# Kernel tuning notes

Measured on AMD Instinct MI355X. Metric: run time of the kernel, lower is better.

## Reference

```python
import jax, jax.numpy as jnp
import numpy as np

B, S, D, H = 2, 2048, 1024, 16
DK = D // H  # 64
THETA = 10000.0
SCALE = 1.0 / np.sqrt(DK)


def _rope(t, pos):
    """Apply rotary embedding. t: [b,h,s,dk], pos: [b,s] int."""
    inv_freq = THETA ** (-jnp.arange(0, DK, 2, dtype=jnp.float32) / DK)  # [dk/2]
    ang = pos[:, None, :, None].astype(jnp.float32) * inv_freq  # [b,1,s,dk/2]
    cos, sin = jnp.cos(ang), jnp.sin(ang)
    t1, t2 = t[..., 0::2], t[..., 1::2]  # interleaved pairs
    rot = jnp.stack([t1 * cos - t2 * sin, t1 * sin + t2 * cos], axis=-1)
    return rot.reshape(t.shape)


def setup_inputs() -> dict:
    key = jax.random.key(0)
    ks = jax.random.split(key, 9)
    sc = 0.02
    x = jax.random.normal(ks[0], (B, S, D), jnp.float32)
    token_position = jnp.tile(jnp.arange(S, dtype=jnp.int32)[None, :], (B, 1))
    Wq = jax.random.normal(ks[1], (D, D), jnp.float32) * sc
    Wk = jax.random.normal(ks[2], (D, D), jnp.float32) * sc
    Wv = jax.random.normal(ks[3], (D, D), jnp.float32) * sc
    Wo = jax.random.normal(ks[4], (D, D), jnp.float32) * sc
    bq = jnp.zeros((D,), jnp.float32)
    bk = jnp.zeros((D,), jnp.float32)
    bv = jnp.zeros((D,), jnp.float32)
    bo = jnp.zeros((D,), jnp.float32)
    return {"x": x, "token_position": token_position,
            "Wq": Wq, "bq": bq, "Wk": Wk, "bk": bk,
            "Wv": Wv, "bv": bv, "Wo": Wo, "bo": bo}


def reference(x, token_position, Wq, bq, Wk, bk, Wv, bv, Wo, bo):
    b, s, d = x.shape
    # projections, split heads: [b,s,d] -> [b,h,s,dk]
    def heads(t):
        return t.reshape(b, s, H, DK).transpose(0, 2, 1, 3)
    q = heads(x @ Wq + bq)
    k = heads(x @ Wk + bk)
    v = heads(x @ Wv + bv)
    q = _rope(q, token_position)
    k = _rope(k, token_position)
    scores = jnp.einsum('bhnk,bhmk->bhnm', q, k) * SCALE  # [b,h,s,s]
    causal = jnp.tril(jnp.ones((s, s), dtype=bool))
    scores = jnp.where(causal, scores, -jnp.inf)
    probs = jax.nn.softmax(scores, axis=-1)
    o = jnp.einsum('bhnm,bhmk->bhnk', probs, v)  # [b,h,s,dk]
    o = o.transpose(0, 2, 1, 3).reshape(b, s, d)
    return o @ Wo + bo
```

## Files before the change

kernel.cpp:

```cpp
#include <hip/hip_runtime.h>
#include <math.h>

#define BB  2
#define SS  2048
#define DD  1024
#define HH  16
#define DKK 64

constexpr float kScale = 0.125f;
constexpr float kC1 = 0.18033688011112042f;
constexpr float kC2 = 23.0831206542234144f;

typedef __bf16 bf16x8 __attribute__((ext_vector_type(8)));
typedef __bf16 bf16x4 __attribute__((ext_vector_type(4)));
typedef float f32x4 __attribute__((ext_vector_type(4)));

__device__ __forceinline__ void async_copy16(const void* g, void* l) {
  __builtin_amdgcn_global_load_lds(
      (const __attribute__((address_space(1))) void*)g,
      (__attribute__((address_space(3))) void*)l, 16, 0, 0);
}

__global__ __launch_bounds__(256) void prep_kernel(
    const float* __restrict__ x, const int* __restrict__ pos,
    const float* __restrict__ W0, const float* __restrict__ W1,
    const float* __restrict__ W2, const float* __restrict__ W3,
    __bf16* __restrict__ xb, float2* __restrict__ rtab,
    __bf16* __restrict__ T0, __bf16* __restrict__ T1,
    __bf16* __restrict__ T2, __bf16* __restrict__ T3) {
  __shared__ __bf16 tile[64][65];
  const int bid = blockIdx.x;
  const int t = threadIdx.x;
  if (bid < 2048) {
    const size_t i = ((size_t)bid * 256 + t) * 8;
    const float4 v0 = *(const float4*)(x + i);
    const float4 v1 = *(const float4*)(x + i + 4);
    bf16x8 o;
    o[0] = (__bf16)v0.x; o[1] = (__bf16)v0.y; o[2] = (__bf16)v0.z; o[3] = (__bf16)v0.w;
    o[4] = (__bf16)v1.x; o[5] = (__bf16)v1.y; o[6] = (__bf16)v1.z; o[7] = (__bf16)v1.w;
    *(bf16x8*)(xb + i) = o;
  } else if (bid < 2560) {
    const int idx = (bid - 2048) * 256 + t;
    const int m = idx >> 5, pi = idx & 31;
    const float inv = exp2f(-0.4152410118609203f * (float)pi);
    float sn, cs;
    __sincosf((float)pos[m] * inv, &sn, &cs);
    rtab[idx] = make_float2(cs, sn);
  } else {
    const int tid2 = bid - 2560;
    const int z = tid2 >> 8, rem = tid2 & 255;
    const float* W;
    __bf16* T;
    switch (z) {
      case 0: W = W0; T = T0; break;
      case 1: W = W1; T = T1; break;
      case 2: W = W2; T = T2; break;
      default: W = W3; T = T3; break;
    }
    const int k0 = (rem >> 4) * 64, n0 = (rem & 15) * 64;
    const int c = t & 63, rg = t >> 6;
#pragma unroll
    for (int i = 0; i < 16; i++) {
      const int r = rg + i * 4;
      tile[r][c] = (__bf16)W[(size_t)(k0 + r) * DD + n0 + c];
    }
    __syncthreads();
#pragma unroll
    for (int i = 0; i < 16; i++) {
      const int r = rg + i * 4;
      T[(size_t)(n0 + r) * DD + k0 + c] = tile[c][r];
    }
  }
}

__device__ __forceinline__ void gemm_core(
    const __bf16* __restrict__ A, const __bf16* __restrict__ Bt,
    int bm, int bn, f32x4 (&acc)[4][4], __bf16* As, __bf16* Bs) {
  const int t = threadIdx.x;
  const int lane = t & 63, wave = t >> 6;
  const int col = lane & 15, quad = lane >> 4;
  const int wm = (wave & 1) * 64, wn = (wave >> 1) * 64;
  const int r8 = lane >> 3;
  const int cg = (lane & 7) ^ r8;
  const __bf16* ag = A + (size_t)(bm + wave * 32 + r8) * DD + cg * 8;
  const __bf16* bg = Bt + (size_t)(bn + wave * 32 + r8) * DD + cg * 8;
  __bf16* asb = As + wave * 32 * 64;
  __bf16* bsb = Bs + wave * 32 * 64;

  for (int kt = 0; kt < DD; kt += 64) {
#pragma unroll
    for (int c = 0; c < 4; c++) {
      async_copy16(ag + (size_t)c * 8 * DD + kt, asb + c * 512);
      async_copy16(bg + (size_t)c * 8 * DD + kt, bsb + c * 512);
    }
    __syncthreads();
#pragma unroll
    for (int ks = 0; ks < 2; ks++) {
      bf16x8 af[4], bf[4];
#pragma unroll
      for (int i = 0; i < 4; i++)
        af[i] = *(const bf16x8*)(As + (wm + i * 16 + col) * 64 +
                                 (((ks * 4 + quad) ^ (col & 7)) * 8));
#pragma unroll
      for (int j = 0; j < 4; j++)
        bf[j] = *(const bf16x8*)(Bs + (wn + j * 16 + col) * 64 +
                                 (((ks * 4 + quad) ^ (col & 7)) * 8));
#pragma unroll
      for (int i = 0; i < 4; i++)
#pragma unroll
        for (int j = 0; j < 4; j++)
          acc[i][j] =
              __builtin_amdgcn_mfma_f32_16x16x32_bf16(af[i], bf[j], acc[i][j], 0, 0, 0);
    }
    __syncthreads();
  }
}

__global__ __launch_bounds__(256) void qkv_gemm_kernel(
    const __bf16* __restrict__ xb, const __bf16* __restrict__ WqT,
    const __bf16* __restrict__ WkT, const __bf16* __restrict__ WvT,
    const float* __restrict__ bq, const float* __restrict__ bk,
    const float* __restrict__ bv, const float2* __restrict__ ropetab,
    __bf16* __restrict__ qo, __bf16* __restrict__ ko, __bf16* __restrict__ vo) {
  __shared__ __bf16 As[128 * 64];
  __shared__ __bf16 Bs[128 * 64];
  const int mat = blockIdx.x >> 3;
  const int bn = (blockIdx.x & 7) * 128;
  const int bm = blockIdx.y * 128;

  f32x4 acc[4][4] = {};
  const int t = threadIdx.x, lane = t & 63, wave = t >> 6;
  const int col = lane & 15, quad = lane >> 4;
  const int wm = (wave & 1) * 64, wn = (wave >> 1) * 64;

  if (mat == 2) {
    gemm_core(WvT, xb, bn, bm, acc, As, Bs);
    const int b = bm >> 11;
#pragma unroll
    for (int i = 0; i < 4; i++) {
#pragma unroll
      for (int r = 0; r < 4; r++) {
        const int n = bn + wm + i * 16 + quad * 4 + r;
        const float bb = bv[n];
        const int h = n >> 6, dk = n & 63;
        __bf16* vrow = vo + ((size_t)(b * HH + h) * DKK + dk) * SS;
#pragma unroll
        for (int j = 0; j < 4; j++) {
          const int m = bm + wn + j * 16 + col;
          vrow[m & (SS - 1)] = (__bf16)(acc[i][j][r] + bb);
        }
      }
    }
    return;
  }

  const __bf16* Bt = mat == 0 ? WqT : WkT;
  const float* bias = mat == 0 ? bq : bk;
  __bf16* out = mat == 0 ? qo : ko;
  gemm_core(xb, Bt, bm, bn, acc, As, Bs);

#pragma unroll
  for (int i = 0; i < 4; i++) {
#pragma unroll
    for (int j = 0; j < 4; j++) {
      const int n = bn + wn + j * 16 + col;
      const float bb = bias[n];
      const int pi = (n & 63) >> 1;
#pragma unroll
      for (int r = 0; r < 4; r++) {
        const int m = bm + wm + i * 16 + quad * 4 + r;
        float v = acc[i][j][r] + bb;
        {
          const float other = __shfl_xor(v, 1, 64);
          const float2 cssn = ropetab[(size_t)m * 32 + pi];
          v = (n & 1) ? (other * cssn.y + v * cssn.x)
                      : (v * cssn.x - other * cssn.y);
        }
        const int h = n >> 6, dk = n & 63;
        const int b = m >> 11, s = m & (SS - 1);
        out[((size_t)(b * HH + h) * SS + s) * DKK + dk] = (__bf16)v;
      }
    }
  }
}

__global__ __launch_bounds__(256) void oproj_gemm_kernel(
    const __bf16* __restrict__ ob, const __bf16* __restrict__ WoT,
    const float* __restrict__ bo, float* __restrict__ out) {
  __shared__ __bf16 As[128 * 64];
  __shared__ __bf16 Bs[128 * 64];
  const int bn = blockIdx.x * 128;
  const int bm = blockIdx.y * 128;
  f32x4 acc[4][4] = {};
  gemm_core(ob, WoT, bm, bn, acc, As, Bs);

  const int t = threadIdx.x, lane = t & 63, wave = t >> 6;
  const int col = lane & 15, quad = lane >> 4;
  const int wm = (wave & 1) * 64, wn = (wave >> 1) * 64;
#pragma unroll
  for (int i = 0; i < 4; i++) {
#pragma unroll
    for (int j = 0; j < 4; j++) {
      const int n = bn + wn + j * 16 + col;
      const float bb = bo[n];
#pragma unroll
      for (int r = 0; r < 4; r++) {
        const int m = bm + wm + i * 16 + quad * 4 + r;
        out[(size_t)m * DD + n] = acc[i][j][r] + bb;
      }
    }
  }
}

__global__ __launch_bounds__(512, 4) void flash_attn_mfma_kernel(
    const __bf16* __restrict__ q, const __bf16* __restrict__ k,
    const __bf16* __restrict__ vt, __bf16* __restrict__ o) {
  __shared__ __bf16 Ks[2][64 * 64];
  __shared__ __bf16 Vs[2][64 * 64];
  __shared__ __bf16 Ps[8][16 * 72];

  const int bh = blockIdx.x;
  const int qtile = 15 - blockIdx.y;
  const int t = threadIdx.x, lane = t & 63, wave = t >> 6;
  const int col = lane & 15, quad = lane >> 4;
  const int r8 = lane >> 3;
  const int cg = (lane & 7) ^ r8;
  const int w4 = wave & 3;

  const __bf16* qb = q + (size_t)bh * SS * DKK;
  const __bf16* kb = k + (size_t)bh * SS * DKK;
  const __bf16* vtb = vt + (size_t)bh * DKK * SS;
  const int b = bh / HH, h = bh % HH;
  __bf16* pw = (__bf16*)Ps[wave];

  const int rbase = qtile * 128 + wave * 16;
  const int myDiag = 2 * qtile + (wave >> 2);
  const int nTiles = 2 * qtile + 2;

  bf16x8 qf[2];
#pragma unroll
  for (int ks = 0; ks < 2; ks++)
    qf[ks] = *(const bf16x8*)(qb + (size_t)(rbase + col) * DKK + ks * 32 +
                              quad * 8);

  f32x4 oacc[4] = {};
  float l_lane = 0.f;

  auto stage = [&](int kt, int buf) {
    async_copy16(kb + (size_t)(kt * 64 + wave * 8 + r8) * DKK + cg * 8,
                 &Ks[buf][wave * 512]);
    async_copy16(vtb + (size_t)(wave * 8 + r8) * SS + kt * 64 + cg * 8,
                 &Vs[buf][wave * 512]);
  };

  stage(0, 0);
  __syncthreads();

  int cur = 0;
  for (int kt = 0; kt < nTiles; kt++) {
    if (kt + 1 < nTiles) stage(kt + 1, cur ^ 1);

    if (kt <= myDiag) {
      f32x4 sc[4] = {};
      __builtin_amdgcn_s_setprio(1);
#pragma unroll
      for (int ct = 0; ct < 4; ct++)
#pragma unroll
        for (int ks = 0; ks < 2; ks++) {
          const bf16x8 kf = *(const bf16x8*)(&Ks[cur][(ct * 16 + col) * 64 +
                                             (((ks * 4 + quad) ^ (col & 7)) * 8)]);
          sc[ct] = __builtin_amdgcn_mfma_f32_16x16x32_bf16(kf, qf[ks], sc[ct],
                                                           0, 0, 0);
        }
      __builtin_amdgcn_s_setprio(0);

      if (kt < myDiag) {
#pragma unroll
        for (int ct = 0; ct < 4; ct++) {
          float p0 = exp2f(sc[ct][0] * kC1 - kC2);
          float p1 = exp2f(sc[ct][1] * kC1 - kC2);
          float p2 = exp2f(sc[ct][2] * kC1 - kC2);
          float p3 = exp2f(sc[ct][3] * kC1 - kC2);
          l_lane += (p0 + p1) + (p2 + p3);
          bf16x4 pv;
          pv[0] = (__bf16)p0; pv[1] = (__bf16)p1;
          pv[2] = (__bf16)p2; pv[3] = (__bf16)p3;
          *(bf16x4*)(pw + col * 72 + ct * 16 + quad * 4) = pv;
        }
      } else {
#pragma unroll
        for (int ct = 0; ct < 4; ct++) {
          bf16x4 pv;
          if (ct > w4) {
            pv[0] = pv[1] = pv[2] = pv[3] = (__bf16)0.0f;
          } else if (ct < w4) {
            float p0 = exp2f(sc[ct][0] * kC1 - kC2);
            float p1 = exp2f(sc[ct][1] * kC1 - kC2);
            float p2 = exp2f(sc[ct][2] * kC1 - kC2);
            float p3 = exp2f(sc[ct][3] * kC1 - kC2);
            l_lane += (p0 + p1) + (p2 + p3);
            pv[0] = (__bf16)p0; pv[1] = (__bf16)p1;
            pv[2] = (__bf16)p2; pv[3] = (__bf16)p3;
          } else {
#pragma unroll
            for (int r = 0; r < 4; r++) {
              float p = exp2f(sc[ct][r] * kC1 - kC2);
              if (quad * 4 + r > col) p = 0.0f;
              l_lane += p;
              pv[r] = (__bf16)p;
            }
          }
          *(bf16x4*)(pw + col * 72 + ct * 16 + quad * 4) = pv;
        }
      }

      {
        bf16x8 pf[2];
#pragma unroll
        for (int ks = 0; ks < 2; ks++)
          pf[ks] = *(const bf16x8*)(pw + col * 72 + ks * 32 + quad * 8);
        __builtin_amdgcn_s_setprio(1);
#pragma unroll
        for (int dt = 0; dt < 4; dt++)
#pragma unroll
          for (int ks = 0; ks < 2; ks++) {
            const bf16x8 vf = *(const bf16x8*)(&Vs[cur][(dt * 16 + col) * 64 +
                                               (((ks * 4 + quad) ^ (col & 7)) * 8)]);
            oacc[dt] = __builtin_amdgcn_mfma_f32_16x16x32_bf16(pf[ks], vf,
                                                               oacc[dt], 0, 0, 0);
          }
        __builtin_amdgcn_s_setprio(0);
      }
    }

    __syncthreads();
    cur ^= 1;
  }

  float l = l_lane;
  l += __shfl_xor(l, 16, 64);
  l += __shfl_xor(l, 32, 64);
#pragma unroll
  for (int r = 0; r < 4; r++) {
    const float lr = __shfl(l, quad * 4 + r, 64);
    const float inv_l = 1.0f / lr;
    const int s = rbase + quad * 4 + r;
#pragma unroll
    for (int dt = 0; dt < 4; dt++)
      o[((size_t)(b * SS + s) * HH + h) * DKK + dt * 16 + col] =
          (__bf16)(oacc[dt][r] * inv_l);
  }
}

extern "C" void kernel_launch(void* const* d_in, const int* in_sizes, int n_in,
                              void* d_out, int out_size, void* d_ws,
                              size_t ws_size, hipStream_t stream) {
  const float* x  = (const float*)d_in[0];
  const int*  pos = (const int*)d_in[1];
  const float* Wq = (const float*)d_in[2];
  const float* bq = (const float*)d_in[3];
  const float* Wk = (const float*)d_in[4];
  const float* bk = (const float*)d_in[5];
  const float* Wv = (const float*)d_in[6];
  const float* bv = (const float*)d_in[7];
  const float* Wo = (const float*)d_in[8];
  const float* bo = (const float*)d_in[9];
  float* out = (float*)d_out;

  char* ws = (char*)d_ws;
  __bf16* xb  = (__bf16*)(ws);
  __bf16* WqT = (__bf16*)(ws + ((size_t)8  << 20));
  __bf16* WkT = (__bf16*)(ws + ((size_t)10 << 20));
  __bf16* WvT = (__bf16*)(ws + ((size_t)12 << 20));
  __bf16* WoT = (__bf16*)(ws + ((size_t)14 << 20));
  __bf16* qb  = (__bf16*)(ws + ((size_t)16 << 20));
  __bf16* kb  = (__bf16*)(ws + ((size_t)24 << 20));
  __bf16* vtb = (__bf16*)(ws + ((size_t)32 << 20));
  __bf16* ob  = (__bf16*)(ws + ((size_t)40 << 20));
  float2* rtab = (float2*)(ws + ((size_t)48 << 20));

  prep_kernel<<<3584, 256, 0, stream>>>(x, pos, Wq, Wk, Wv, Wo, xb, rtab, WqT,
                                        WkT, WvT, WoT);
  qkv_gemm_kernel<<<dim3(24, 32), 256, 0, stream>>>(xb, WqT, WkT, WvT, bq, bk,
                                                    bv, rtab, qb, kb, vtb);
  flash_attn_mfma_kernel<<<dim3(32, 16), 512, 0, stream>>>(qb, kb, vtb, ob);
  oproj_gemm_kernel<<<dim3(8, 32), 256, 0, stream>>>(ob, WoT, bo, out);
}
```

Measured before the change: 199.1 us.

## Double-buffer GEMM K-tiles in LDS with async prefetch of next tile

Changes the shared GEMM core from single-buffered 64-wide K tiles to double-buffered 32-wide K tiles, issuing the async global-to-LDS copy for the next tile before computing the current one. This cuts the synchronisations per K step from two to one and is meant to overlap load latency with MFMA work. It also changes the XOR swizzle to suit 32-column rows and raises wave priority around the MFMA block. The risk is that the halved K depth per barrier adds loop overhead. It also relies on the async copies completing before the single barrier.

```diff
diff --git a/kernel.cpp b/kernel.cpp
--- a/kernel.cpp
+++ b/kernel.cpp
@@ -80,39 +80,51 @@
   const int lane = t & 63, wave = t >> 6;
   const int col = lane & 15, quad = lane >> 4;
   const int wm = (wave & 1) * 64, wn = (wave >> 1) * 64;
-  const int r8 = lane >> 3;
-  const int cg = (lane & 7) ^ r8;
-  const __bf16* ag = A + (size_t)(bm + wave * 32 + r8) * DD + cg * 8;
-  const __bf16* bg = Bt + (size_t)(bn + wave * 32 + r8) * DD + cg * 8;
-  __bf16* asb = As + wave * 32 * 64;
-  __bf16* bsb = Bs + wave * 32 * 64;
-
-  for (int kt = 0; kt < DD; kt += 64) {
-#pragma unroll
-    for (int c = 0; c < 4; c++) {
-      async_copy16(ag + (size_t)c * 8 * DD + kt, asb + c * 512);
-      async_copy16(bg + (size_t)c * 8 * DD + kt, bsb + c * 512);
-    }
+
+  const int r16 = lane >> 2;
+  const int gch = (lane & 3) ^ ((r16 >> 1) & 3);
+  const __bf16* ag = A + (size_t)(bm + wave * 32 + r16) * DD + gch * 8;
+  const __bf16* bg = Bt + (size_t)(bn + wave * 32 + r16) * DD + gch * 8;
+  __bf16* asb = As + wave * 1024;
+  __bf16* bsb = Bs + wave * 1024;
+
+  const int rch = (quad ^ ((col >> 1) & 3)) * 8;
+
+  auto stage = [&](int kt, int buf) {
+    const int bo = buf * 4096;
+    async_copy16(ag + kt, asb + bo);
+    async_copy16(ag + (size_t)16 * DD + kt, asb + bo + 512);
+    async_copy16(bg + kt, bsb + bo);
+    async_copy16(bg + (size_t)16 * DD + kt, bsb + bo + 512);
+  };
+
+  stage(0, 0);
+  __syncthreads();
+
+  int cur = 0;
+#pragma unroll 2
+  for (int step = 0; step < 32; step++) {
+    if (step + 1 < 32) stage((step + 1) * 32, cur ^ 1);
+
+    const int bo = cur * 4096;
+    bf16x8 af[4], bf[4];
+#pragma unroll
+    for (int i = 0; i < 4; i++)
+      af[i] = *(const bf16x8*)(As + bo + (wm + i * 16 + col) * 32 + rch);
+#pragma unroll
+    for (int j = 0; j < 4; j++)
+      bf[j] = *(const bf16x8*)(Bs + bo + (wn + j * 16 + col) * 32 + rch);
+    __builtin_amdgcn_s_setprio(1);
+#pragma unroll
+    for (int i = 0; i < 4; i++)
+#pragma unroll
+      for (int j = 0; j < 4; j++)
+        acc[i][j] =
+            __builtin_amdgcn_mfma_f32_16x16x32_bf16(af[i], bf[j], acc[i][j], 0, 0, 0);
+    __builtin_amdgcn_s_setprio(0);
+
     __syncthreads();
-#pragma unroll
-    for (int ks = 0; ks < 2; ks++) {
-      bf16x8 af[4], bf[4];
-#pragma unroll
-      for (int i = 0; i < 4; i++)
-        af[i] = *(const bf16x8*)(As + (wm + i * 16 + col) * 64 +
-                                 (((ks * 4 + quad) ^ (col & 7)) * 8));
-#pragma unroll
-      for (int j = 0; j < 4; j++)
-        bf[j] = *(const bf16x8*)(Bs + (wn + j * 16 + col) * 64 +
-                                 (((ks * 4 + quad) ^ (col & 7)) * 8));
-#pragma unroll
-      for (int i = 0; i < 4; i++)
-#pragma unroll
-        for (int j = 0; j < 4; j++)
-          acc[i][j] =
-              __builtin_amdgcn_mfma_f32_16x16x32_bf16(af[i], bf[j], acc[i][j], 0, 0, 0);
-    }
-    __syncthreads();
+    cur ^= 1;
   }
 }
 
@@ -122,8 +134,8 @@
     const float* __restrict__ bq, const float* __restrict__ bk,
     const float* __restrict__ bv, const float2* __restrict__ ropetab,
     __bf16* __restrict__ qo, __bf16* __restrict__ ko, __bf16* __restrict__ vo) {
-  __shared__ __bf16 As[128 * 64];
-  __shared__ __bf16 Bs[128 * 64];
+  __shared__ __bf16 As[2 * 128 * 32];
+  __shared__ __bf16 Bs[2 * 128 * 32];
   const int mat = blockIdx.x >> 3;
   const int bn = (blockIdx.x & 7) * 128;
   const int bm = blockIdx.y * 128;
@@ -187,8 +199,8 @@
 __global__ __launch_bounds__(256) void oproj_gemm_kernel(
     const __bf16* __restrict__ ob, const __bf16* __restrict__ WoT,
     const float* __restrict__ bo, float* __restrict__ out) {
-  __shared__ __bf16 As[128 * 64];
-  __shared__ __bf16 Bs[128 * 64];
+  __shared__ __bf16 As[2 * 128 * 32];
+  __shared__ __bf16 Bs[2 * 128 * 32];
   const int bn = blockIdx.x * 128;
   const int bm = blockIdx.y * 128;
   f32x4 acc[4][4] = {};
```

New measurement: 210.9 us. 5.9% more time.
